# Optimization experiments

Hardware: AMD Instinct MI355X
Metric: run time of the kernel (lower is better)

Reference implementation:

```python
import jax, jax.numpy as jnp
import numpy as np

N, LQ, DM = 8, 2500, 256
NH, NL, NP, NZ = 8, 4, 8, 4
DH = DM // NH
SPATIAL = np.array([[64, 176], [32, 88], [16, 44], [8, 22]], dtype=np.int32)
LEN_IN = int((SPATIAL[:, 0] * SPATIAL[:, 1]).sum())


def setup_inputs() -> dict:
    key = jax.random.key(0)
    ks = jax.random.split(key, 10)
    query = jax.random.normal(ks[0], (N, LQ, DM), dtype=jnp.float32)
    query_pos = jax.random.normal(ks[1], (N, LQ, DM), dtype=jnp.float32)
    reference_points = jax.random.uniform(ks[2], (N, LQ, NZ, 2), dtype=jnp.float32)
    input_flatten = jax.random.normal(ks[3], (N, LEN_IN, DM), dtype=jnp.float32)
    input_spatial_shapes = jnp.asarray(SPATIAL)
    lsi = np.concatenate([[0], np.cumsum(SPATIAL[:, 0] * SPATIAL[:, 1])[:-1]]).astype(np.int32)
    input_level_start_index = jnp.asarray(lsi)
    # learned params (Linear: y = x @ W + b, W is (in, out))
    Wv = jax.random.normal(ks[4], (DM, DM), dtype=jnp.float32) * (1.0 / np.sqrt(DM))
    bv = jnp.zeros((DM,), dtype=jnp.float32)
    Wo = jax.random.normal(ks[5], (DM, NH * NL * NP * 2), dtype=jnp.float32) * 0.02
    bo = jax.random.normal(ks[6], (NH * NL * NP * 2,), dtype=jnp.float32) * 1.0
    Wa = jax.random.normal(ks[7], (DM, NH * NL * NP), dtype=jnp.float32) * 0.02
    ba = jnp.zeros((NH * NL * NP,), dtype=jnp.float32)
    return {"query": query, "query_pos": query_pos, "reference_points": reference_points,
            "input_flatten": input_flatten, "input_spatial_shapes": input_spatial_shapes,
            "input_level_start_index": input_level_start_index,
            "Wv": Wv, "bv": bv, "Wo": Wo, "bo": bo, "Wa": Wa, "ba": ba}


def _sample_level(v, h, w, loc):
    """Bilinear sample (grid_sample, align_corners=False, zero padding).
    v:   (N, h*w, NH, DH) level feature map
    loc: (N, Lq, NH, P, 2) normalized locations in [0,1] (x, y)
    returns (N, NH, Lq, P, DH)
    """
    n, hw, nh, dh = v.shape
    lq, p = loc.shape[1], loc.shape[3]
    x = loc[..., 0] * w - 0.5
    y = loc[..., 1] * h - 0.5
    x0f = jnp.floor(x)
    y0f = jnp.floor(y)
    wx = x - x0f
    wy = y - y0f
    x0 = x0f.astype(jnp.int32)
    y0 = y0f.astype(jnp.int32)
    vt = v.transpose(0, 2, 1, 3).reshape(n * nh, hw, dh)

    def gather(xi, yi, wgt):
        valid = ((xi >= 0) & (xi < w) & (yi >= 0) & (yi < h)).astype(v.dtype)
        idx = jnp.clip(yi, 0, h - 1) * w + jnp.clip(xi, 0, w - 1)  # (N,Lq,NH,P)
        idx = idx.transpose(0, 2, 1, 3).reshape(n * nh, lq * p)
        g = jnp.take_along_axis(vt, idx[:, :, None], axis=1)  # (N*NH, Lq*P, DH)
        wv = (wgt * valid).transpose(0, 2, 1, 3).reshape(n * nh, lq * p)
        return g * wv[:, :, None]

    out = (gather(x0, y0, (1 - wx) * (1 - wy))
           + gather(x0 + 1, y0, wx * (1 - wy))
           + gather(x0, y0 + 1, (1 - wx) * wy)
           + gather(x0 + 1, y0 + 1, wx * wy))
    return out.reshape(n, nh, lq, p, dh)


def _forward(query, query_pos, reference_points, input_flatten, spatial, Wv, bv, Wo, bo, Wa, ba):
    n, lq, _ = query.shape
    len_in = input_flatten.shape[1]
    # projections
    value = (input_flatten @ Wv + bv).reshape(n, len_in, NH, DH)
    off = (query @ Wo + bo).reshape(n, lq, NH, NL, NP, 2)
    aw = jax.nn.softmax((query @ Wa + ba).reshape(n, lq, NH, NL * NP), axis=-1)
    aw = aw.reshape(n, lq, NH, NL, NP)
    # normalize offsets by (W_l, H_l), add to Z-anchor reference points
    norm = jnp.asarray(np.stack([spatial[:, 1], spatial[:, 0]], -1), dtype=query.dtype)  # (NL,2)
    off = off / norm[None, None, None, :, None, :]
    off = off.reshape(n, lq, NH, NL, NP // NZ, NZ, 2)
    ref = reference_points[:, :, None, None, None, :, :]  # (N,Lq,1,1,1,NZ,2)
    loc = (ref + off).reshape(n, lq, NH, NL, NP, 2)
    # multi-scale deformable sampling + weighted reduction
    out = jnp.zeros((n, lq, NH, DH), dtype=query.dtype)
    start = 0
    for lvl in range(NL):
        h, w = int(spatial[lvl, 0]), int(spatial[lvl, 1])
        v_l = value[:, start:start + h * w]
        start += h * w
        samp = _sample_level(v_l, h, w, loc[:, :, :, lvl])  # (N,NH,Lq,NP,DH)
        out = out + jnp.einsum('nhqpd,nqhp->nqhd', samp, aw[:, :, :, lvl])
    return out.reshape(n, lq, DM)


def reference(query, query_pos, reference_points, input_flatten, input_spatial_shapes,
              input_level_start_index, Wv, bv, Wo, bo, Wa, ba):
    spatial = np.asarray(jax.device_get(input_spatial_shapes))
    return _forward(query, query_pos, reference_points, input_flatten, spatial,
                    Wv, bv, Wo, bo, Wa, ba)
```

## Files before the change

### kernel.cpp

```cpp
#include <hip/hip_runtime.h>
#include <hip/hip_fp16.h>

#define N_BATCH 8
#define LQ_     2500
#define DM_     256
#define NH_     8
#define NL_     4
#define NP_     8
#define DH_     32
#define LEN_IN_ 14960
#define KDIM    256

__constant__ int c_w[4]     = {176, 88, 44, 22};
__constant__ int c_h[4]     = {64, 32, 16, 8};
__constant__ int c_start[4] = {0, 11264, 14080, 14784};

using bf16x8 = __attribute__((ext_vector_type(8))) short;
using f32x4  = __attribute__((ext_vector_type(4))) float;

static __device__ inline void split_bf16(float v, unsigned short& hi, unsigned short& lo) {
    unsigned int u = __float_as_uint(v);
    hi = (unsigned short)(u >> 16);
    float hif = __uint_as_float(u & 0xFFFF0000u);
    float l = v - hif;
    lo = (unsigned short)(__float_as_uint(l) >> 16);
}

static __device__ inline unsigned short f2bf_rne(float v) {
    unsigned int u = __float_as_uint(v);
    u += 0x7FFFu + ((u >> 16) & 1u);
    return (unsigned short)(u >> 16);
}

__global__ __launch_bounds__(256) void conv_weights(
    const float* __restrict__ Wv, const float* __restrict__ Wo,
    const float* __restrict__ Wa, const float* __restrict__ bo,
    const float* __restrict__ ba,
    unsigned short* __restrict__ Wv_hi, unsigned short* __restrict__ Wv_lo,
    unsigned short* __restrict__ Wc_hi, unsigned short* __restrict__ Wc_lo,
    float* __restrict__ bcomb)
{
    int id = blockIdx.x * 256 + threadIdx.x;
    if (id < 256 * 256) {
        int n = id >> 8, k = id & 255;
        unsigned short h, l;
        split_bf16(Wv[k * 256 + n], h, l);
        Wv_hi[id] = h; Wv_lo[id] = l;
    } else {
        int id2 = id - 65536;
        if (id2 < 768 * 256) {
            int n = id2 >> 8, k = id2 & 255;
            float v = (n < 512) ? Wo[k * 512 + n] : Wa[k * 256 + (n - 512)];
            unsigned short h, l;
            split_bf16(v, h, l);
            Wc_hi[id2] = h; Wc_lo[id2] = l;
        }
    }
    if (id < 768) bcomb[id] = (id < 512) ? bo[id] : ba[id - 512];
}

template <bool BF16_OUT, bool XSWIZ>
__global__ __launch_bounds__(512, 4) void gemm_mfma2(
    const float* __restrict__ A,
    const unsigned short* __restrict__ Bt_hi,
    const unsigned short* __restrict__ Bt_lo,
    const float* __restrict__ bias,
    float* __restrict__ C,
    unsigned short* __restrict__ Cb,
    int M, int N, int nbm)
{
    __shared__ unsigned short As[128][40];
    __shared__ unsigned short Bh[128][40];
    __shared__ unsigned short Bl[128][40];

    const int tid  = threadIdx.x;
    const int ntn  = N >> 7;
    int by, bx;
    if (XSWIZ) {
        int xcd = blockIdx.x & 7, j = blockIdx.x >> 3;
        by = xcd + 8 * (j / ntn);
        bx = j % ntn;
        if (by >= nbm) return;
    } else {
        by = blockIdx.x / ntn;
        bx = blockIdx.x % ntn;
    }
    const int row0 = by << 7, col0 = bx << 7;
    const int lane = tid & 63, wave = tid >> 6;
    const int wrow = (wave & 1) << 6, wcol = (wave >> 1) << 5;
    const int r16  = lane & 15, quad = lane >> 4;

    const int ar0 = tid >> 3;
    const int ac4 = (tid & 7) << 2;
    const int bn  = tid >> 2;
    const int bg  = (tid & 3) << 3;

    float4 pa[2];
    uint4  pbh, pbl;

#pragma unroll
    for (int i = 0; i < 2; ++i) {
        int row = row0 + ar0 + (i << 6);
        pa[i] = (row < M) ? *(const float4*)&A[(size_t)row * KDIM + ac4]
                          : make_float4(0.f, 0.f, 0.f, 0.f);
    }
    {
        size_t goff = (size_t)(col0 + bn) * KDIM + bg;
        pbh = *(const uint4*)&Bt_hi[goff];
        pbl = *(const uint4*)&Bt_lo[goff];
    }

    f32x4 acc[4][2];
#pragma unroll
    for (int i = 0; i < 4; ++i)
#pragma unroll
        for (int j = 0; j < 2; ++j) acc[i][j] = (f32x4){0.f, 0.f, 0.f, 0.f};

#pragma unroll
    for (int kt = 0; kt < KDIM; kt += 32) {
#pragma unroll
        for (int i = 0; i < 2; ++i) {
            int r = ar0 + (i << 6);
            ushort4 hv;
            hv.x = f2bf_rne(pa[i].x);
            hv.y = f2bf_rne(pa[i].y);
            hv.z = f2bf_rne(pa[i].z);
            hv.w = f2bf_rne(pa[i].w);
            *(ushort4*)&As[r][ac4] = hv;
        }
        *(uint4*)&Bh[bn][bg] = pbh;
        *(uint4*)&Bl[bn][bg] = pbl;
        __syncthreads();

        if (kt + 32 < KDIM) {
#pragma unroll
            for (int i = 0; i < 2; ++i) {
                int row = row0 + ar0 + (i << 6);
                pa[i] = (row < M)
                    ? *(const float4*)&A[(size_t)row * KDIM + kt + 32 + ac4]
                    : make_float4(0.f, 0.f, 0.f, 0.f);
            }
            size_t goff = (size_t)(col0 + bn) * KDIM + kt + 32 + bg;
            pbh = *(const uint4*)&Bt_hi[goff];
            pbl = *(const uint4*)&Bt_lo[goff];
        }

        bf16x8 fbh[2], fbl[2], fa[4];
#pragma unroll
        for (int tn = 0; tn < 2; ++tn) {
            int n = wcol + tn * 16 + r16;
            fbh[tn] = *(const bf16x8*)&Bh[n][quad << 3];
            fbl[tn] = *(const bf16x8*)&Bl[n][quad << 3];
        }
#pragma unroll
        for (int tm = 0; tm < 4; ++tm)
            fa[tm] = *(const bf16x8*)&As[wrow + tm * 16 + r16][quad << 3];
#pragma unroll
        for (int tm = 0; tm < 4; ++tm)
#pragma unroll
            for (int tn = 0; tn < 2; ++tn) {
                acc[tm][tn] = __builtin_amdgcn_mfma_f32_16x16x32_bf16(fa[tm], fbl[tn], acc[tm][tn], 0, 0, 0);
                acc[tm][tn] = __builtin_amdgcn_mfma_f32_16x16x32_bf16(fa[tm], fbh[tn], acc[tm][tn], 0, 0, 0);
            }
        __syncthreads();
    }

    float bvs[2];
#pragma unroll
    for (int tn = 0; tn < 2; ++tn) bvs[tn] = bias[col0 + wcol + tn * 16 + r16];
#pragma unroll
    for (int tm = 0; tm < 4; ++tm) {
#pragma unroll
        for (int i = 0; i < 4; ++i) {
            int row = row0 + wrow + tm * 16 + (quad << 2) + i;
            if (row < M) {
                if (!BF16_OUT) {
                    float* crow = C + (size_t)row * N + col0 + wcol + r16;
#pragma unroll
                    for (int tn = 0; tn < 2; ++tn)
                        crow[tn * 16] = acc[tm][tn][i] + bvs[tn];
                } else {
                    int n   = row / LEN_IN_;
                    int pix = row - n * LEN_IN_;
#pragma unroll
                    for (int tn = 0; tn < 2; ++tn) {
                        int col = col0 + wcol + tn * 16 + r16;
                        int h = col >> 5, dh = col & 31;
                        size_t addr = ((size_t)(n * NH_ + h) * LEN_IN_ + pix) * DH_ + dh;
                        Cb[addr] = f2bf_rne(acc[tm][tn][i] + bvs[tn]);
                    }
                }
            }
        }
    }
}

__global__ __launch_bounds__(256) void ms_sample(
    const unsigned short* __restrict__ value,
    const float* __restrict__ comb,
    const float* __restrict__ ref_pts,
    float* __restrict__ out)
{
    __shared__ uint4 s_desc[64][33];

    const int b     = blockIdx.x;
    const int xcd   = b & 7;
    const int j     = b >> 3;
    const int slice = (j / 40) * 8 + xcd;
    const int chunk = j % 40;
    const int n     = slice >> 3, h = slice & 7;
    const int q0    = chunk * 64;
    const int tid   = threadIdx.x;

    {
        int ql = tid >> 2, l = tid & 3;
        int q  = q0 + ql;
        if (q < LQ_) {
            int nq = n * LQ_ + q;
            const float* row = comb + (size_t)nq * 768;

            float4 L0 = *(const float4*)&row[512 + h * 32 + l * 8];
            float4 L1 = *(const float4*)&row[512 + h * 32 + l * 8 + 4];
            float lg[8] = {L0.x, L0.y, L0.z, L0.w, L1.x, L1.y, L1.z, L1.w};
            float m = lg[0];
#pragma unroll
            for (int i = 1; i < 8; ++i) m = fmaxf(m, lg[i]);
            m = fmaxf(m, __shfl_xor(m, 1));
            m = fmaxf(m, __shfl_xor(m, 2));
            float e[8], s = 0.f;
#pragma unroll
            for (int i = 0; i < 8; ++i) { e[i] = __expf(lg[i] - m); s += e[i]; }
            s += __shfl_xor(s, 1);
            s += __shfl_xor(s, 2);
            float inv = 1.f / s;

            float4 R0 = *(const float4*)&ref_pts[(size_t)nq * 8];
            float4 R1 = *(const float4*)&ref_pts[(size_t)nq * 8 + 4];
            float rx[4] = {R0.x, R0.z, R1.x, R1.z};
            float ry[4] = {R0.y, R0.w, R1.y, R1.w};

            float off[16];
#pragma unroll
            for (int i = 0; i < 4; ++i)
                *(float4*)&off[i * 4] = *(const float4*)&row[h * 64 + l * 16 + i * 4];

            float wl = (float)c_w[l], hl = (float)c_h[l];
            int wli = c_w[l], hli = c_h[l], st = c_start[l];
#pragma unroll
            for (int p = 0; p < 8; ++p) {
                int z = p & 3;
                float a = e[p] * inv;
                float x = rx[z] * wl + off[p * 2 + 0] - 0.5f;
                float y = ry[z] * hl + off[p * 2 + 1] - 0.5f;
                float x0f = floorf(x), y0f = floorf(y);
                int   x0 = (int)x0f,  y0 = (int)y0f;
                float wx = x - x0f,   wy = y - y0f;
                unsigned short ix[4];
                float wt[4];
#pragma unroll
                for (int jj = 0; jj < 4; ++jj) {
                    int xi = x0 + (jj & 1);
                    int yi = y0 + (jj >> 1);
                    float w = ((jj & 1) ? wx : 1.f - wx) * ((jj >> 1) ? wy : 1.f - wy);
                    bool valid = (xi >= 0) && (xi < wli) && (yi >= 0) && (yi < hli);
                    int xc = min(max(xi, 0), wli - 1);
                    int yc = min(max(yi, 0), hli - 1);
                    ix[jj] = (unsigned short)(yc * wli + xc);
                    wt[jj] = valid ? a * w : 0.f;
                }
                uint4 d;
                d.x = (unsigned int)(st + ix[0]) | ((unsigned int)(st + ix[1]) << 16);
                d.y = (unsigned int)(st + ix[2]) | ((unsigned int)(st + ix[3]) << 16);
                __half2 h01 = __floats2half2_rn(wt[0], wt[1]);
                __half2 h23 = __floats2half2_rn(wt[2], wt[3]);
                d.z = *(unsigned int*)&h01;
                d.w = *(unsigned int*)&h23;
                s_desc[ql][l * 8 + p] = d;
            }
        }
    }
    __syncthreads();

    int ql = tid >> 2, dhg = tid & 3;
    int q  = q0 + ql;
    if (q >= LQ_) return;
    int nq = n * LQ_ + q;
    const unsigned short* vb = value
        + ((size_t)(n * NH_ + h) * LEN_IN_) * DH_ + dhg * 8;

    float acc[8];
#pragma unroll
    for (int i = 0; i < 8; ++i) acc[i] = 0.f;

#pragma unroll 2
    for (int s = 0; s < 32; ++s) {
        uint4 d = s_desc[ql][s];
        float2 w01 = __half22float2(*(const __half2*)&d.z);
        float2 w23 = __half22float2(*(const __half2*)&d.w);
        int i0 = d.x & 0xFFFF, i1 = d.x >> 16;
        int i2 = d.y & 0xFFFF, i3 = d.y >> 16;
        uint4 v0 = *(const uint4*)(vb + i0 * DH_);
        uint4 v1 = *(const uint4*)(vb + i1 * DH_);
        uint4 v2 = *(const uint4*)(vb + i2 * DH_);
        uint4 v3 = *(const uint4*)(vb + i3 * DH_);
        const uint4* vv[4] = {&v0, &v1, &v2, &v3};
        float ww[4] = {w01.x, w01.y, w23.x, w23.y};
#pragma unroll
        for (int c = 0; c < 4; ++c) {
            uint4 v = *vv[c];
            float w = ww[c];
            acc[0] = fmaf(__uint_as_float(v.x << 16), w, acc[0]);
            acc[1] = fmaf(__uint_as_float(v.x & 0xFFFF0000u), w, acc[1]);
            acc[2] = fmaf(__uint_as_float(v.y << 16), w, acc[2]);
            acc[3] = fmaf(__uint_as_float(v.y & 0xFFFF0000u), w, acc[3]);
            acc[4] = fmaf(__uint_as_float(v.z << 16), w, acc[4]);
            acc[5] = fmaf(__uint_as_float(v.z & 0xFFFF0000u), w, acc[5]);
            acc[6] = fmaf(__uint_as_float(v.w << 16), w, acc[6]);
            acc[7] = fmaf(__uint_as_float(v.w & 0xFFFF0000u), w, acc[7]);
        }
    }

    float* op = out + (size_t)nq * 256 + h * 32 + dhg * 8;
    *(float4*)&op[0] = make_float4(acc[0], acc[1], acc[2], acc[3]);
    *(float4*)&op[4] = make_float4(acc[4], acc[5], acc[6], acc[7]);
}

extern "C" void kernel_launch(void* const* d_in, const int* in_sizes, int n_in,
                              void* d_out, int out_size, void* d_ws, size_t ws_size,
                              hipStream_t stream)
{
    const float* query         = (const float*)d_in[0];
    const float* ref_pts       = (const float*)d_in[2];
    const float* input_flatten = (const float*)d_in[3];
    const float* Wv            = (const float*)d_in[6];
    const float* bv            = (const float*)d_in[7];
    const float* Wo            = (const float*)d_in[8];
    const float* bo            = (const float*)d_in[9];
    const float* Wa            = (const float*)d_in[10];
    const float* ba            = (const float*)d_in[11];
    float* out = (float*)d_out;

    char* ws = (char*)d_ws;
    size_t o = 0;
    unsigned short* Wv_hi = (unsigned short*)(ws + o); o += 256 * 256 * 2;
    unsigned short* Wv_lo = (unsigned short*)(ws + o); o += 256 * 256 * 2;
    unsigned short* Wc_hi = (unsigned short*)(ws + o); o += 768 * 256 * 2;
    unsigned short* Wc_lo = (unsigned short*)(ws + o); o += 768 * 256 * 2;
    float*          bcomb = (float*)(ws + o);          o += 768 * 4;
    o = (o + 511) & ~(size_t)511;
    unsigned short* value = (unsigned short*)(ws + o); o += (size_t)119680 * 256 * 2;
    o = (o + 511) & ~(size_t)511;
    float* combq = (float*)(ws + o); o += (size_t)20000 * 768 * 4;

    const int MV = N_BATCH * LEN_IN_;
    const int MQ = N_BATCH * LQ_;

    hipLaunchKernelGGL(conv_weights, dim3(1024), dim3(256), 0, stream,
                       Wv, Wo, Wa, bo, ba, Wv_hi, Wv_lo, Wc_hi, Wc_lo, bcomb);
    hipLaunchKernelGGL((gemm_mfma2<true, false>), dim3((MV / 128) * 2), dim3(512), 0, stream,
                       input_flatten, Wv_hi, Wv_lo, bv, (float*)nullptr, value, MV, 256, 0);
    hipLaunchKernelGGL((gemm_mfma2<false, true>), dim3(8 * 20 * 6), dim3(512), 0, stream,
                       query, Wc_hi, Wc_lo, bcomb, combq, (unsigned short*)nullptr, MQ, 768, 157);
    hipLaunchKernelGGL(ms_sample, dim3(2560), dim3(256), 0, stream,
                       value, combq, ref_pts, out);
}
```

Baseline: 368.3 us.

## Fuse value and query projection GEMMs into one launch with deeper prefetch

Merges the two separate projection GEMMs (value projection and offset/attention projection) into a single kernel whose grid interleaves blocks of both problems. Every third block goes to the query GEMM, so both GEMMs can fill the device together and one launch and tail are removed. It also double-buffers the global prefetch two k-steps ahead and rearranges shared memory into k-group-major [4][128][8] tiles to change LDS bank access. Row bounds are now handled by clamping the row index instead of branching, which adds some register pressure.

```diff
diff --git a/kernel.cpp b/kernel.cpp
--- a/kernel.cpp
+++ b/kernel.cpp
@@ -11,6 +11,11 @@
 #define LEN_IN_ 14960
 #define KDIM    256
 
+#define MV_   119680
+#define MQ_   20000
+#define NBMV  935
+#define NBMQ  157
+
 __constant__ int c_w[4]     = {176, 88, 44, 22};
 __constant__ int c_h[4]     = {64, 32, 16, 8};
 __constant__ int c_start[4] = {0, 11264, 14080, 14784};
@@ -30,6 +35,15 @@
     unsigned int u = __float_as_uint(v);
     u += 0x7FFFu + ((u >> 16) & 1u);
     return (unsigned short)(u >> 16);
+}
+
+static __device__ inline ushort4 cvt4_rne(float4 v) {
+    ushort4 h;
+    h.x = f2bf_rne(v.x);
+    h.y = f2bf_rne(v.y);
+    h.z = f2bf_rne(v.z);
+    h.w = f2bf_rne(v.w);
+    return h;
 }
 
 __global__ __launch_bounds__(256) void conv_weights(
@@ -59,32 +73,46 @@
     if (id < 768) bcomb[id] = (id < 512) ? bo[id] : ba[id - 512];
 }
 
-template <bool BF16_OUT, bool XSWIZ>
-__global__ __launch_bounds__(512, 4) void gemm_mfma2(
-    const float* __restrict__ A,
-    const unsigned short* __restrict__ Bt_hi,
-    const unsigned short* __restrict__ Bt_lo,
-    const float* __restrict__ bias,
-    float* __restrict__ C,
-    unsigned short* __restrict__ Cb,
-    int M, int N, int nbm)
+__global__ __launch_bounds__(512, 4) void gemm_fused(
+    const float* __restrict__ Av,
+    const float* __restrict__ Aq,
+    const unsigned short* __restrict__ Wvh, const unsigned short* __restrict__ Wvl,
+    const unsigned short* __restrict__ Wch, const unsigned short* __restrict__ Wcl,
+    const float* __restrict__ bv, const float* __restrict__ bcomb,
+    float* __restrict__ Cq,
+    unsigned short* __restrict__ Cv)
 {
-    __shared__ unsigned short As[128][40];
-    __shared__ unsigned short Bh[128][40];
-    __shared__ unsigned short Bl[128][40];
-
-    const int tid  = threadIdx.x;
-    const int ntn  = N >> 7;
-    int by, bx;
-    if (XSWIZ) {
-        int xcd = blockIdx.x & 7, j = blockIdx.x >> 3;
-        by = xcd + 8 * (j / ntn);
-        bx = j % ntn;
-        if (by >= nbm) return;
+    __shared__ unsigned short As[4][128][8];
+    __shared__ unsigned short Bh[4][128][8];
+    __shared__ unsigned short Bl[4][128][8];
+
+    const int tid = threadIdx.x;
+    const int bid = blockIdx.x;
+    const int g   = bid / 3;
+    const int r3  = bid - 3 * g;
+
+    const float* A;
+    const unsigned short *Bth, *Btl;
+    const float* bias;
+    int M, N, by, bx;
+    bool v_out;
+    if (r3 == 2) {
+        int c = g;
+        int xcd = bid & 7, j = c >> 3;
+        int jq = j / 6;
+        by = xcd + 8 * jq;
+        bx = j - 6 * jq;
+        if (by >= NBMQ) return;
+        A = Aq; Bth = Wch; Btl = Wcl; bias = bcomb;
+        M = MQ_; N = 768; v_out = false;
     } else {
-        by = blockIdx.x / ntn;
-        bx = blockIdx.x % ntn;
-    }
+        int v = 2 * g + r3;
+        by = v >> 1; bx = v & 1;
+        if (by >= NBMV) return;
+        A = Av; Bth = Wvh; Btl = Wvl; bias = bv;
+        M = MV_; N = 256; v_out = true;
+    }
+
     const int row0 = by << 7, col0 = bx << 7;
     const int lane = tid & 63, wave = tid >> 6;
     const int wrow = (wave & 1) << 6, wcol = (wave >> 1) << 5;
@@ -92,22 +120,23 @@
 
     const int ar0 = tid >> 3;
     const int ac4 = (tid & 7) << 2;
+    const int ag  = ac4 >> 3;
+    const int ae  = ac4 & 7;
     const int bn  = tid >> 2;
-    const int bg  = (tid & 3) << 3;
-
-    float4 pa[2];
-    uint4  pbh, pbl;
-
-#pragma unroll
-    for (int i = 0; i < 2; ++i) {
-        int row = row0 + ar0 + (i << 6);
-        pa[i] = (row < M) ? *(const float4*)&A[(size_t)row * KDIM + ac4]
-                          : make_float4(0.f, 0.f, 0.f, 0.f);
-    }
-    {
-        size_t goff = (size_t)(col0 + bn) * KDIM + bg;
-        pbh = *(const uint4*)&Bt_hi[goff];
-        pbl = *(const uint4*)&Bt_lo[goff];
+    const int bgr = tid & 3;
+
+    const size_t arow0 = (size_t)min(row0 + ar0,      M - 1) * KDIM;
+    const size_t arow1 = (size_t)min(row0 + ar0 + 64, M - 1) * KDIM;
+    const size_t boff  = (size_t)(col0 + bn) * KDIM + (bgr << 3);
+
+    float4 pa[2][2];
+    uint4  pbh[2], pbl[2];
+#pragma unroll
+    for (int s = 0; s < 2; ++s) {
+        pa[s][0] = *(const float4*)&A[arow0 + s * 32 + ac4];
+        pa[s][1] = *(const float4*)&A[arow1 + s * 32 + ac4];
+        pbh[s]   = *(const uint4*)&Bth[boff + s * 32];
+        pbl[s]   = *(const uint4*)&Btl[boff + s * 32];
     }
 
     f32x4 acc[4][2];
@@ -117,44 +146,33 @@
         for (int j = 0; j < 2; ++j) acc[i][j] = (f32x4){0.f, 0.f, 0.f, 0.f};
 
 #pragma unroll
-    for (int kt = 0; kt < KDIM; kt += 32) {
-#pragma unroll
-        for (int i = 0; i < 2; ++i) {
-            int r = ar0 + (i << 6);
-            ushort4 hv;
-            hv.x = f2bf_rne(pa[i].x);
-            hv.y = f2bf_rne(pa[i].y);
-            hv.z = f2bf_rne(pa[i].z);
-            hv.w = f2bf_rne(pa[i].w);
-            *(ushort4*)&As[r][ac4] = hv;
-        }
-        *(uint4*)&Bh[bn][bg] = pbh;
-        *(uint4*)&Bl[bn][bg] = pbl;
+    for (int kt = 0; kt < 8; ++kt) {
+        const int cur = kt & 1;
+
+        *(ushort4*)&As[ag][ar0][ae]      = cvt4_rne(pa[cur][0]);
+        *(ushort4*)&As[ag][ar0 + 64][ae] = cvt4_rne(pa[cur][1]);
+        *(uint4*)&Bh[bgr][bn][0] = pbh[cur];
+        *(uint4*)&Bl[bgr][bn][0] = pbl[cur];
         __syncthreads();
 
-        if (kt + 32 < KDIM) {
-#pragma unroll
-            for (int i = 0; i < 2; ++i) {
-                int row = row0 + ar0 + (i << 6);
-                pa[i] = (row < M)
-                    ? *(const float4*)&A[(size_t)row * KDIM + kt + 32 + ac4]
-                    : make_float4(0.f, 0.f, 0.f, 0.f);
-            }
-            size_t goff = (size_t)(col0 + bn) * KDIM + kt + 32 + bg;
-            pbh = *(const uint4*)&Bt_hi[goff];
-            pbl = *(const uint4*)&Bt_lo[goff];
+        if (kt < 6) {
+            const int k0 = (kt + 2) * 32;
+            pa[cur][0] = *(const float4*)&A[arow0 + k0 + ac4];
+            pa[cur][1] = *(const float4*)&A[arow1 + k0 + ac4];
+            pbh[cur]   = *(const uint4*)&Bth[boff + k0];
+            pbl[cur]   = *(const uint4*)&Btl[boff + k0];
         }
 
         bf16x8 fbh[2], fbl[2], fa[4];
 #pragma unroll
         for (int tn = 0; tn < 2; ++tn) {
             int n = wcol + tn * 16 + r16;
-            fbh[tn] = *(const bf16x8*)&Bh[n][quad << 3];
-            fbl[tn] = *(const bf16x8*)&Bl[n][quad << 3];
+            fbh[tn] = *(const bf16x8*)&Bh[quad][n][0];
+            fbl[tn] = *(const bf16x8*)&Bl[quad][n][0];
         }
 #pragma unroll
         for (int tm = 0; tm < 4; ++tm)
-            fa[tm] = *(const bf16x8*)&As[wrow + tm * 16 + r16][quad << 3];
+            fa[tm] = *(const bf16x8*)&As[quad][wrow + tm * 16 + r16][0];
 #pragma unroll
         for (int tm = 0; tm < 4; ++tm)
 #pragma unroll
@@ -174,8 +192,8 @@
         for (int i = 0; i < 4; ++i) {
             int row = row0 + wrow + tm * 16 + (quad << 2) + i;
             if (row < M) {
-                if (!BF16_OUT) {
-                    float* crow = C + (size_t)row * N + col0 + wcol + r16;
+                if (!v_out) {
+                    float* crow = Cq + (size_t)row * N + col0 + wcol + r16;
 #pragma unroll
                     for (int tn = 0; tn < 2; ++tn)
                         crow[tn * 16] = acc[tm][tn][i] + bvs[tn];
@@ -187,7 +205,7 @@
                         int col = col0 + wcol + tn * 16 + r16;
                         int h = col >> 5, dh = col & 31;
                         size_t addr = ((size_t)(n * NH_ + h) * LEN_IN_ + pix) * DH_ + dh;
-                        Cb[addr] = f2bf_rne(acc[tm][tn][i] + bvs[tn]);
+                        Cv[addr] = f2bf_rne(acc[tm][tn][i] + bvs[tn]);
                     }
                 }
             }
@@ -352,15 +370,11 @@
     o = (o + 511) & ~(size_t)511;
     float* combq = (float*)(ws + o); o += (size_t)20000 * 768 * 4;
 
-    const int MV = N_BATCH * LEN_IN_;
-    const int MQ = N_BATCH * LQ_;
-
     hipLaunchKernelGGL(conv_weights, dim3(1024), dim3(256), 0, stream,
                        Wv, Wo, Wa, bo, ba, Wv_hi, Wv_lo, Wc_hi, Wc_lo, bcomb);
-    hipLaunchKernelGGL((gemm_mfma2<true, false>), dim3((MV / 128) * 2), dim3(512), 0, stream,
-                       input_flatten, Wv_hi, Wv_lo, bv, (float*)nullptr, value, MV, 256, 0);
-    hipLaunchKernelGGL((gemm_mfma2<false, true>), dim3(8 * 20 * 6), dim3(512), 0, stream,
-                       query, Wc_hi, Wc_lo, bcomb, combq, (unsigned short*)nullptr, MQ, 768, 157);
+    hipLaunchKernelGGL(gemm_fused, dim3(2880), dim3(512), 0, stream,
+                       input_flatten, query, Wv_hi, Wv_lo, Wc_hi, Wc_lo,
+                       bv, bcomb, combq, value);
     hipLaunchKernelGGL(ms_sample, dim3(2560), dim3(256), 0, stream,
                        value, combq, ref_pts, out);
 }
```

Result: slower. 408.3 us (+10.9%).

## Pre-cast GEMM activations to bf16 and stream tiles via global_load_lds

Applied to the files above, without the earlier changes.

Adds a separate cast kernel that converts input_flatten and query to bf16. The results are stored in buffers that reuse the combq workspace and the output buffer. Both projection GEMMs are rewritten to copy A and the hi/lo weight tiles straight from global memory into LDS with global_load_lds, which removes the per-element conversion and register staging from the GEMM loop. Occupancy bounds are also raised. The trade-off is an extra full read and write pass over the activations, the loss of the register-prefetch overlap of the next K tile, and an unpadded LDS layout that may cause bank conflicts.

```diff
diff --git a/kernel.cpp b/kernel.cpp
--- a/kernel.cpp
+++ b/kernel.cpp
@@ -11,12 +11,21 @@
 #define LEN_IN_ 14960
 #define KDIM    256
 
+#define MV_   119680
+#define MQ_   20000
+#define NBMQ  157
+
 __constant__ int c_w[4]     = {176, 88, 44, 22};
 __constant__ int c_h[4]     = {64, 32, 16, 8};
 __constant__ int c_start[4] = {0, 11264, 14080, 14784};
 
 using bf16x8 = __attribute__((ext_vector_type(8))) short;
 using f32x4  = __attribute__((ext_vector_type(4))) float;
+
+#define GLDS16(g, l)                                                         \
+    __builtin_amdgcn_global_load_lds(                                        \
+        (const __attribute__((address_space(1))) void*)(g),                  \
+        (__attribute__((address_space(3))) void*)(l), 16, 0, 0)
 
 static __device__ inline void split_bf16(float v, unsigned short& hi, unsigned short& lo) {
     unsigned int u = __float_as_uint(v);
@@ -30,6 +39,29 @@
     unsigned int u = __float_as_uint(v);
     u += 0x7FFFu + ((u >> 16) & 1u);
     return (unsigned short)(u >> 16);
+}
+
+static __device__ inline ushort4 cvt4_rne(float4 v) {
+    ushort4 h;
+    h.x = f2bf_rne(v.x);
+    h.y = f2bf_rne(v.y);
+    h.z = f2bf_rne(v.z);
+    h.w = f2bf_rne(v.w);
+    return h;
+}
+
+__global__ __launch_bounds__(256) void cast_bf16(
+    const float* __restrict__ src, unsigned short* __restrict__ dst, int n8)
+{
+    const float4* s = (const float4*)src;
+    ushort4*      d = (ushort4*)dst;
+    int i = blockIdx.x * 256 + threadIdx.x;
+    const int st = gridDim.x * 256;
+    for (; i < n8; i += st) {
+        float4 a = s[2 * i], b = s[2 * i + 1];
+        d[2 * i]     = cvt4_rne(a);
+        d[2 * i + 1] = cvt4_rne(b);
+    }
 }
 
 __global__ __launch_bounds__(256) void conv_weights(
@@ -60,21 +92,21 @@
 }
 
 template <bool BF16_OUT, bool XSWIZ>
-__global__ __launch_bounds__(512, 4) void gemm_mfma2(
-    const float* __restrict__ A,
-    const unsigned short* __restrict__ Bt_hi,
-    const unsigned short* __restrict__ Bt_lo,
+__global__ __launch_bounds__(512, 6) void gemm_glds(
+    const unsigned short* __restrict__ Abf,
+    const unsigned short* __restrict__ Bth,
+    const unsigned short* __restrict__ Btl,
     const float* __restrict__ bias,
     float* __restrict__ C,
     unsigned short* __restrict__ Cb,
     int M, int N, int nbm)
 {
-    __shared__ unsigned short As[128][40];
-    __shared__ unsigned short Bh[128][40];
-    __shared__ unsigned short Bl[128][40];
-
-    const int tid  = threadIdx.x;
-    const int ntn  = N >> 7;
+    __shared__ __align__(16) unsigned short As [4096];
+    __shared__ __align__(16) unsigned short Bhs[4096];
+    __shared__ __align__(16) unsigned short Bls[4096];
+
+    const int tid = threadIdx.x;
+    const int ntn = N >> 7;
     int by, bx;
     if (XSWIZ) {
         int xcd = blockIdx.x & 7, j = blockIdx.x >> 3;
@@ -82,33 +114,22 @@
         bx = j % ntn;
         if (by >= nbm) return;
     } else {
-        by = blockIdx.x / ntn;
-        bx = blockIdx.x % ntn;
+        by = blockIdx.x >> 1;
+        bx = blockIdx.x & 1;
     }
     const int row0 = by << 7, col0 = bx << 7;
     const int lane = tid & 63, wave = tid >> 6;
     const int wrow = (wave & 1) << 6, wcol = (wave >> 1) << 5;
     const int r16  = lane & 15, quad = lane >> 4;
 
-    const int ar0 = tid >> 3;
-    const int ac4 = (tid & 7) << 2;
-    const int bn  = tid >> 2;
-    const int bg  = (tid & 3) << 3;
-
-    float4 pa[2];
-    uint4  pbh, pbl;
-
-#pragma unroll
-    for (int i = 0; i < 2; ++i) {
-        int row = row0 + ar0 + (i << 6);
-        pa[i] = (row < M) ? *(const float4*)&A[(size_t)row * KDIM + ac4]
-                          : make_float4(0.f, 0.f, 0.f, 0.f);
-    }
-    {
-        size_t goff = (size_t)(col0 + bn) * KDIM + bg;
-        pbh = *(const uint4*)&Bt_hi[goff];
-        pbl = *(const uint4*)&Bt_lo[goff];
-    }
+    const int srow = tid >> 2, skq = tid & 3;
+    const int arow = min(row0 + srow, M - 1);
+    const unsigned short* gA  = Abf + (size_t)arow * KDIM + skq * 8;
+    const unsigned short* gBh = Bth + (size_t)(col0 + srow) * KDIM + skq * 8;
+    const unsigned short* gBl = Btl + (size_t)(col0 + srow) * KDIM + skq * 8;
+    unsigned short* lA  = &As [wave << 9];
+    unsigned short* lBh = &Bhs[wave << 9];
+    unsigned short* lBl = &Bls[wave << 9];
 
     f32x4 acc[4][2];
 #pragma unroll
@@ -117,44 +138,22 @@
         for (int j = 0; j < 2; ++j) acc[i][j] = (f32x4){0.f, 0.f, 0.f, 0.f};
 
 #pragma unroll
-    for (int kt = 0; kt < KDIM; kt += 32) {
-#pragma unroll
-        for (int i = 0; i < 2; ++i) {
-            int r = ar0 + (i << 6);
-            ushort4 hv;
-            hv.x = f2bf_rne(pa[i].x);
-            hv.y = f2bf_rne(pa[i].y);
-            hv.z = f2bf_rne(pa[i].z);
-            hv.w = f2bf_rne(pa[i].w);
-            *(ushort4*)&As[r][ac4] = hv;
-        }
-        *(uint4*)&Bh[bn][bg] = pbh;
-        *(uint4*)&Bl[bn][bg] = pbl;
+    for (int kt = 0; kt < 8; ++kt) {
+        GLDS16(gA  + kt * 32, lA);
+        GLDS16(gBh + kt * 32, lBh);
+        GLDS16(gBl + kt * 32, lBl);
         __syncthreads();
-
-        if (kt + 32 < KDIM) {
-#pragma unroll
-            for (int i = 0; i < 2; ++i) {
-                int row = row0 + ar0 + (i << 6);
-                pa[i] = (row < M)
-                    ? *(const float4*)&A[(size_t)row * KDIM + kt + 32 + ac4]
-                    : make_float4(0.f, 0.f, 0.f, 0.f);
-            }
-            size_t goff = (size_t)(col0 + bn) * KDIM + kt + 32 + bg;
-            pbh = *(const uint4*)&Bt_hi[goff];
-            pbl = *(const uint4*)&Bt_lo[goff];
-        }
 
         bf16x8 fbh[2], fbl[2], fa[4];
 #pragma unroll
         for (int tn = 0; tn < 2; ++tn) {
             int n = wcol + tn * 16 + r16;
-            fbh[tn] = *(const bf16x8*)&Bh[n][quad << 3];
-            fbl[tn] = *(const bf16x8*)&Bl[n][quad << 3];
+            fbh[tn] = *(const bf16x8*)&Bhs[n * 32 + (quad << 3)];
+            fbl[tn] = *(const bf16x8*)&Bls[n * 32 + (quad << 3)];
         }
 #pragma unroll
         for (int tm = 0; tm < 4; ++tm)
-            fa[tm] = *(const bf16x8*)&As[wrow + tm * 16 + r16][quad << 3];
+            fa[tm] = *(const bf16x8*)&As[(wrow + tm * 16 + r16) * 32 + (quad << 3)];
 #pragma unroll
         for (int tm = 0; tm < 4; ++tm)
 #pragma unroll
@@ -352,15 +351,19 @@
     o = (o + 511) & ~(size_t)511;
     float* combq = (float*)(ws + o); o += (size_t)20000 * 768 * 4;
 
-    const int MV = N_BATCH * LEN_IN_;
-    const int MQ = N_BATCH * LQ_;
+    unsigned short* Abf_v = (unsigned short*)combq;
+    unsigned short* Abf_q = (unsigned short*)d_out;
 
     hipLaunchKernelGGL(conv_weights, dim3(1024), dim3(256), 0, stream,
                        Wv, Wo, Wa, bo, ba, Wv_hi, Wv_lo, Wc_hi, Wc_lo, bcomb);
-    hipLaunchKernelGGL((gemm_mfma2<true, false>), dim3((MV / 128) * 2), dim3(512), 0, stream,
-                       input_flatten, Wv_hi, Wv_lo, bv, (float*)nullptr, value, MV, 256, 0);
-    hipLaunchKernelGGL((gemm_mfma2<false, true>), dim3(8 * 20 * 6), dim3(512), 0, stream,
-                       query, Wc_hi, Wc_lo, bcomb, combq, (unsigned short*)nullptr, MQ, 768, 157);
+    hipLaunchKernelGGL(cast_bf16, dim3(2048), dim3(256), 0, stream,
+                       input_flatten, Abf_v, MV_ * KDIM / 8);
+    hipLaunchKernelGGL(cast_bf16, dim3(1024), dim3(256), 0, stream,
+                       query, Abf_q, MQ_ * KDIM / 8);
+    hipLaunchKernelGGL((gemm_glds<true, false>), dim3((MV_ / 128) * 2), dim3(512), 0, stream,
+                       Abf_v, Wv_hi, Wv_lo, bv, (float*)nullptr, value, MV_, 256, 0);
+    hipLaunchKernelGGL((gemm_glds<false, true>), dim3(8 * 20 * 6), dim3(512), 0, stream,
+                       Abf_q, Wc_hi, Wc_lo, bcomb, combq, (unsigned short*)nullptr, MQ_, 768, NBMQ);
     hipLaunchKernelGGL(ms_sample, dim3(2560), dim3(256), 0, stream,
                        value, combq, ref_pts, out);
 }
```

After: 376.0 us. 1.02x slower.
